# Performance work log

Measured on AMD Instinct MI355X. Metric: run time of the kernel, lower is better.

The kernel has to match this reference:

```python
import jax, jax.numpy as jnp
import numpy as np

B, N, E = 4, 1024, 16
S = 4  # num species
AH = PH = 64  # hidden dims


def _mlp(x, W0, b0, W1, b1, W2, b2):
    h = jax.nn.silu(x @ W0 + b0)
    h = jax.nn.silu(h @ W1 + b1)
    return h @ W2 + b2  # [..., 1]


def setup_inputs() -> dict:
    key = jax.random.key(0)
    ks = jax.random.split(key, 20)
    scale = 0.1
    inp = {
        "positions": jax.random.normal(ks[0], (B, N, 2), jnp.float32),
        "species": jax.random.randint(ks[1], (B, N), 0, S, jnp.int32),
        "electric_field": jax.random.normal(ks[2], (B, 2), jnp.float32),
        "embed": jax.random.normal(ks[3], (S, E), jnp.float32) * scale,
        "aW0": jax.random.normal(ks[4], (2 + 2 + 1 + E, AH), jnp.float32) * scale,
        "ab0": jax.random.normal(ks[5], (AH,), jnp.float32) * scale,
        "aW1": jax.random.normal(ks[6], (AH, AH), jnp.float32) * scale,
        "ab1": jax.random.normal(ks[7], (AH,), jnp.float32) * scale,
        "aW2": jax.random.normal(ks[8], (AH, 1), jnp.float32) * scale,
        "ab2": jax.random.normal(ks[9], (1,), jnp.float32) * scale,
        "pW0": jax.random.normal(ks[10], (2 + 1 + 1 + 1 + 2 * E, PH), jnp.float32) * scale,
        "pb0": jax.random.normal(ks[11], (PH,), jnp.float32) * scale,
        "pW1": jax.random.normal(ks[12], (PH, PH), jnp.float32) * scale,
        "pb1": jax.random.normal(ks[13], (PH,), jnp.float32) * scale,
        "pW2": jax.random.normal(ks[14], (PH, 1), jnp.float32) * scale,
        "pb2": jax.random.normal(ks[15], (1,), jnp.float32) * scale,
    }
    return inp


def reference(positions, species, electric_field, embed,
              aW0, ab0, aW1, ab1, aW2, ab2,
              pW0, pb0, pW1, pb1, pW2, pb2):
    num_atoms = positions.shape[1]
    cp = positions - positions.mean(axis=1, keepdims=True)         # [B,N,2]
    semb = embed[species]                                          # [B,N,E]
    e_norm = jnp.linalg.norm(electric_field, axis=-1, keepdims=True)  # [B,1]

    # atom channel
    atom_field = jnp.broadcast_to(electric_field[:, None, :], (cp.shape[0], num_atoms, 2))
    atom_enorm = jnp.broadcast_to(e_norm[:, None, :], (cp.shape[0], num_atoms, 1))
    atom_feat = jnp.concatenate([cp, atom_field, atom_enorm, semb], axis=-1)
    atom_energy = _mlp(atom_feat, aW0, ab0, aW1, ab1, aW2, ab2)[..., 0].sum(axis=1)

    # pair channel: all i<j pairs, fully vectorized
    i_idx, j_idx = jnp.triu_indices(num_atoms, k=1)                # [P]
    rij = cp[:, i_idx, :] - cp[:, j_idx, :]                        # [B,P,2]
    dij = jnp.linalg.norm(rij, axis=-1, keepdims=True)             # [B,P,1]
    uij = rij / jnp.maximum(dij, 1e-12)
    e_dot_u = jnp.sum(electric_field[:, None, :] * uij, axis=-1, keepdims=True)
    pair_enorm = jnp.broadcast_to(e_norm[:, None, :], dij.shape)
    pair_feat = jnp.concatenate(
        [rij, dij, e_dot_u, pair_enorm, semb[:, i_idx, :], semb[:, j_idx, :]], axis=-1)
    pair_energy = _mlp(pair_feat, pW0, pb0, pW1, pb1, pW2, pb2)[..., 0].sum(axis=1)

    return atom_energy + pair_energy
```

## Files before the change

kernel.cpp:

```cpp
#include <hip/hip_runtime.h>

#define NA 1024
#define NBATCH 4
#define NPAIR 523776
#define PAIR_TILES 2046
#define PAIR_BLOCKS 512
#define GRID_X 513

#define WS_MEAN 0
#define WS_W0P  64
#define WS_W0A  4160
#define WS_W1P  8256
#define WS_W1A  16448

typedef _Float16 half8 __attribute__((ext_vector_type(8)));
typedef float float4v __attribute__((ext_vector_type(4)));

__device__ __forceinline__ float silu_f(float x) {
    return x * __builtin_amdgcn_rcpf(1.0f + __expf(-x));
}

__device__ __forceinline__ uint32_t pkf16(float a, float b) {
    union { _Float16 h[2]; uint32_t u; } x;
    x.h[0] = (_Float16)a; x.h[1] = (_Float16)b;
    return x.u;
}

__global__ void prep_kernel(const float* __restrict__ positions,
                            const float* __restrict__ embed,
                            const float* __restrict__ aW0,
                            const float* __restrict__ ab0,
                            const float* __restrict__ aW1,
                            const float* __restrict__ ab2,
                            const float* __restrict__ pW0,
                            const float* __restrict__ pb0,
                            const float* __restrict__ pW1,
                            const float* __restrict__ pb2,
                            char* __restrict__ ws,
                            float* __restrict__ out) {
    const int tid = threadIdx.x;
    if (blockIdx.x < 4) {
        const int b = blockIdx.x;
        const float2* pos = (const float2*)positions + b * NA;
        float sx = 0.f, sy = 0.f;
        for (int t = tid; t < NA; t += 256) {
            float2 p = pos[t];
            sx += p.x; sy += p.y;
        }
#pragma unroll
        for (int off = 32; off > 0; off >>= 1) {
            sx += __shfl_down(sx, off);
            sy += __shfl_down(sy, off);
        }
        __shared__ float rxs[4], rys[4];
        const int w = tid >> 6, lane = tid & 63;
        if (lane == 0) { rxs[w] = sx; rys[w] = sy; }
        __syncthreads();
        if (tid == 0) {
            float* meanws = (float*)(ws + WS_MEAN);
            meanws[b * 2 + 0] = (rxs[0] + rxs[1] + rxs[2] + rxs[3]) * (1.f / NA);
            meanws[b * 2 + 1] = (rys[0] + rys[1] + rys[2] + rys[3]) * (1.f / NA);
            out[b] = (float)NPAIR * pb2[0] + (float)NA * ab2[0];
        }
        return;
    }

    _Float16* w0p = (_Float16*)(ws + WS_W0P);
    _Float16* w0a = (_Float16*)(ws + WS_W0A);
    _Float16* w1p = (_Float16*)(ws + WS_W1P);
    _Float16* w1a = (_Float16*)(ws + WS_W1A);

    for (int idx = tid; idx < 2048; idx += 256) {
        const int j = idx & 7, lane = (idx >> 3) & 63, nt = idx >> 9;
        const int k = ((lane >> 4) << 3) + j;
        const int col = nt * 16 + (lane & 15);
        float vp = 0.f, va = 0.f;
        if (k < 5) {
            vp = pW0[k * 64 + col];
            va = aW0[k * 64 + col];
        } else if (k == 5) {
            vp = pb0[col];
            va = ab0[col];
        } else if (k >= 6 && k <= 9) {
            const int s = k - 6;
            float accp = 0.f, acca = 0.f;
#pragma unroll
            for (int e = 0; e < 16; e++) {
                float em = embed[s * 16 + e];
                accp += em * pW0[(5 + e) * 64 + col];
                acca += em * aW0[(5 + e) * 64 + col];
            }
            vp = accp; va = acca;
        } else if (k >= 10 && k <= 13) {
            const int s = k - 10;
            float accp = 0.f;
#pragma unroll
            for (int e = 0; e < 16; e++)
                accp += embed[s * 16 + e] * pW0[(21 + e) * 64 + col];
            vp = accp; va = 0.f;
        }
        w0p[idx] = (_Float16)vp;
        w0a[idx] = (_Float16)va;
    }
    for (int idx = tid; idx < 4096; idx += 256) {
        const int j = idx & 7, lane = (idx >> 3) & 63;
        const int ks = (idx >> 9) & 1, nt = idx >> 10;
        const int q = lane >> 4;
        const int m = (j < 4) ? (4 * q + j) : (16 + 4 * q + (j - 4));
        const int k = ks * 32 + m;
        const int col = nt * 16 + (lane & 15);
        w1p[idx] = (_Float16)pW1[k * 64 + col];
        w1a[idx] = (_Float16)aW1[k * 64 + col];
    }
}

__global__ __launch_bounds__(256, 4) void mlp_kernel(
    const float* __restrict__ positions,
    const int*   __restrict__ species,
    const float* __restrict__ efield,
    const float* __restrict__ ab1, const float* __restrict__ aW2,
    const float* __restrict__ pb1, const float* __restrict__ pW2,
    const char*  __restrict__ ws,
    float* __restrict__ out)
{
    const int b    = blockIdx.y;
    const int bx   = blockIdx.x;
    const bool is_atom = (bx == PAIR_BLOCKS);
    const int tid  = threadIdx.x;
    const int lane = tid & 63;
    const int wv   = tid >> 6;
    const int n16  = lane & 15;
    const int quad = lane >> 4;

    __shared__ __attribute__((aligned(16))) _Float16 Xbuf[4][64][40];
    _Float16 (*rows)[40] = Xbuf[wv];

    const _Float16* w0w = (const _Float16*)(ws + (is_atom ? WS_W0A : WS_W0P));
    const _Float16* w1w = (const _Float16*)(ws + (is_atom ? WS_W1A : WS_W1P));
    half8 w0f[4], w1f[4][2];
#pragma unroll
    for (int nt = 0; nt < 4; nt++)
        w0f[nt] = *(const half8*)(w0w + (nt * 64 + lane) * 8);
#pragma unroll
    for (int nt = 0; nt < 4; nt++)
#pragma unroll
        for (int ks = 0; ks < 2; ks++)
            w1f[nt][ks] = *(const half8*)(w1w + ((nt * 2 + ks) * 64 + lane) * 8);

    const float* B1 = is_atom ? ab1 : pb1;
    const float* W2 = is_atom ? aW2 : pW2;
    float4v b1q[4], w2q[4];
#pragma unroll
    for (int nt = 0; nt < 4; nt++) {
        b1q[nt] = *(const float4v*)(B1 + nt * 16 + quad * 4);
        w2q[nt] = *(const float4v*)(W2 + nt * 16 + quad * 4);
    }

    *(int4*)&rows[lane][16] = make_int4(0, 0, 0, 0);
    *(int4*)&rows[lane][24] = make_int4(0, 0, 0, 0);

    const float Ex = efield[b * 2 + 0];
    const float Ey = efield[b * 2 + 1];
    const float enorm = sqrtf(Ex * Ex + Ey * Ey);
    const float* meanws = (const float*)(ws + WS_MEAN);

    const int my_tiles = is_atom ? 4 : ((bx < PAIR_TILES - 3 * PAIR_BLOCKS) ? 4 : 3);

    float energy = 0.f;
    for (int t = 0; t < my_tiles; ++t) {
        float f0, f1, f2, f3;
        uint64_t ohi, ohj;
        if (!is_atom) {
            const int tile = bx + t * PAIR_BLOCKS;
            const int p = tile * 256 + tid;
            float Df = (float)(2047 * 2047 - 8 * p);
            int i = (int)((2047.0f - sqrtf(Df)) * 0.5f);
            i = i < 0 ? 0 : (i > 1022 ? 1022 : i);
            while (i * (2047 - i) / 2 > p) --i;
            while ((i + 1) * (2046 - i) / 2 <= p) ++i;
            const int j = p - i * (2047 - i) / 2 + i + 1;
            const float2* pos = (const float2*)positions + b * NA;
            float2 pi = pos[i], pj = pos[j];
            f0 = pi.x - pj.x; f1 = pi.y - pj.y;
            f2 = sqrtf(f0 * f0 + f1 * f1);
            float inv = __builtin_amdgcn_rcpf(fmaxf(f2, 1e-12f));
            f3 = (Ex * f0 + Ey * f1) * inv;
            ohi = 0x3C00ull << (species[b * NA + i] * 16);
            ohj = 0x3C00ull << (species[b * NA + j] * 16);
        } else {
            const int n = t * 256 + tid;
            float2 pn = ((const float2*)positions)[b * NA + n];
            f0 = pn.x - meanws[b * 2 + 0];
            f1 = pn.y - meanws[b * 2 + 1];
            f2 = Ex; f3 = Ey;
            ohi = 0x3C00ull << (species[b * NA + n] * 16);
            ohj = 0;
        }
        int4* dst = (int4*)&rows[lane][0];
        int4 lo, hi;
        lo.x = (int)pkf16(f0, f1);
        lo.y = (int)pkf16(f2, f3);
        lo.z = (int)pkf16(enorm, 1.0f);
        lo.w = (int)(uint32_t)ohi;
        hi.x = (int)(uint32_t)(ohi >> 32);
        hi.y = (int)(uint32_t)ohj;
        hi.z = (int)(uint32_t)(ohj >> 32);
        hi.w = 0;
        dst[0] = lo;
        dst[1] = hi;

#pragma unroll
        for (int mt = 0; mt < 4; mt++) {
            half8 xf = *(const half8*)(&rows[mt * 16 + n16][quad * 8]);

            float4v acc[4];
#pragma unroll
            for (int nt = 0; nt < 4; nt++) {
                float4v z = {0.f, 0.f, 0.f, 0.f};
                acc[nt] = __builtin_amdgcn_mfma_f32_16x16x32_f16(w0f[nt], xf, z, 0, 0, 0);
            }
            half8 h0, h1;
#pragma unroll
            for (int r = 0; r < 4; r++) {
                h0[r]     = (_Float16)silu_f(acc[0][r]);
                h0[4 + r] = (_Float16)silu_f(acc[1][r]);
                h1[r]     = (_Float16)silu_f(acc[2][r]);
                h1[4 + r] = (_Float16)silu_f(acc[3][r]);
            }

#pragma unroll
            for (int nt = 0; nt < 4; nt++) {
                float4v c = b1q[nt];
                c = __builtin_amdgcn_mfma_f32_16x16x32_f16(w1f[nt][0], h0, c, 0, 0, 0);
                c = __builtin_amdgcn_mfma_f32_16x16x32_f16(w1f[nt][1], h1, c, 0, 0, 0);
#pragma unroll
                for (int r = 0; r < 4; r++)
                    energy += silu_f(c[r]) * w2q[nt][r];
            }
        }
    }

#pragma unroll
    for (int off = 32; off > 0; off >>= 1)
        energy += __shfl_down(energy, off);
    __shared__ float wsum[4];
    if (lane == 0) wsum[wv] = energy;
    __syncthreads();
    if (tid == 0)
        atomicAdd(&out[b], wsum[0] + wsum[1] + wsum[2] + wsum[3]);
}

extern "C" void kernel_launch(void* const* d_in, const int* in_sizes, int n_in,
                              void* d_out, int out_size, void* d_ws, size_t ws_size,
                              hipStream_t stream) {
    const float* positions = (const float*)d_in[0];
    const int*   species   = (const int*)  d_in[1];
    const float* efield    = (const float*)d_in[2];
    const float* embed     = (const float*)d_in[3];
    const float* aW0 = (const float*)d_in[4];
    const float* ab0 = (const float*)d_in[5];
    const float* aW1 = (const float*)d_in[6];
    const float* ab1 = (const float*)d_in[7];
    const float* aW2 = (const float*)d_in[8];
    const float* ab2 = (const float*)d_in[9];
    const float* pW0 = (const float*)d_in[10];
    const float* pb0 = (const float*)d_in[11];
    const float* pW1 = (const float*)d_in[12];
    const float* pb1 = (const float*)d_in[13];
    const float* pW2 = (const float*)d_in[14];
    const float* pb2 = (const float*)d_in[15];
    float* outp = (float*)d_out;
    char*  ws   = (char*)d_ws;

    prep_kernel<<<dim3(5), dim3(256), 0, stream>>>(
        positions, embed, aW0, ab0, aW1, ab2, pW0, pb0, pW1, pb2, ws, outp);
    mlp_kernel<<<dim3(GRID_X, NBATCH), dim3(256), 0, stream>>>(
        positions, species, efield,
        ab1, aW2, pb1, pW2,
        ws, outp);
}
```

Before: 169.2 us.

## Shrink layer-0 MFMA to K=16, fold log2e into weights, defer W2 dot

Packs the 14 layer-0 input features into a K=16 fragment and uses the 16x16x16 f16 MFMA, halving layer-0 matrix work, shared-memory row width and weight-prep size. Folds log2(e) into the layer-0 weights and layer-1 bias so SiLU can use a raw exp2, then undoes the scale with ln2 at the end. Defers the multiply by W2 until after the tile loop: each thread keeps per-column SiLU sums and does one dot product at the end, dropping per-element FMAs and registers. The pair grid shrinks to 511 blocks, so two blocks now take 5 tiles instead of 4, which may lengthen the tail; occupancy is pinned with amdgpu_waves_per_eu.

```diff
diff --git a/kernel.cpp b/kernel.cpp
--- a/kernel.cpp
+++ b/kernel.cpp
@@ -4,20 +4,33 @@
 #define NBATCH 4
 #define NPAIR 523776
 #define PAIR_TILES 2046
-#define PAIR_BLOCKS 512
-#define GRID_X 513
+#define PAIR_BLOCKS 511
+#define GRID_X 512
+
+#define LOG2E_F 1.44269504088896f
+#define LN2_F   0.69314718055995f
 
 #define WS_MEAN 0
 #define WS_W0P  64
-#define WS_W0A  4160
-#define WS_W1P  8256
-#define WS_W1A  16448
-
+#define WS_W0A  2112
+#define WS_W1P  4160
+#define WS_W1A  12352
+
+typedef _Float16 half4 __attribute__((ext_vector_type(4)));
 typedef _Float16 half8 __attribute__((ext_vector_type(8)));
 typedef float float4v __attribute__((ext_vector_type(4)));
 
-__device__ __forceinline__ float silu_f(float x) {
-    return x * __builtin_amdgcn_rcpf(1.0f + __expf(-x));
+#if defined(__has_builtin)
+#  if __has_builtin(__builtin_amdgcn_exp2f)
+#    define EXP2F(x) __builtin_amdgcn_exp2f(x)
+#  endif
+#endif
+#ifndef EXP2F
+#  define EXP2F(x) exp2f(x)
+#endif
+
+__device__ __forceinline__ float siluy(float y) {
+    return y * __builtin_amdgcn_rcpf(1.0f + EXP2F(-y));
 }
 
 __device__ __forceinline__ uint32_t pkf16(float a, float b) {
@@ -70,9 +83,9 @@
     _Float16* w1p = (_Float16*)(ws + WS_W1P);
     _Float16* w1a = (_Float16*)(ws + WS_W1A);
 
-    for (int idx = tid; idx < 2048; idx += 256) {
-        const int j = idx & 7, lane = (idx >> 3) & 63, nt = idx >> 9;
-        const int k = ((lane >> 4) << 3) + j;
+    for (int idx = tid; idx < 1024; idx += 256) {
+        const int j = idx & 3, lane = (idx >> 2) & 63, nt = idx >> 8;
+        const int k = ((lane >> 4) << 2) + j;
         const int col = nt * 16 + (lane & 15);
         float vp = 0.f, va = 0.f;
         if (k < 5) {
@@ -99,8 +112,8 @@
                 accp += embed[s * 16 + e] * pW0[(21 + e) * 64 + col];
             vp = accp; va = 0.f;
         }
-        w0p[idx] = (_Float16)vp;
-        w0a[idx] = (_Float16)va;
+        w0p[idx] = (_Float16)(vp * LOG2E_F);
+        w0a[idx] = (_Float16)(va * LOG2E_F);
     }
     for (int idx = tid; idx < 4096; idx += 256) {
         const int j = idx & 7, lane = (idx >> 3) & 63;
@@ -114,7 +127,9 @@
     }
 }
 
-__global__ __launch_bounds__(256, 4) void mlp_kernel(
+__global__ __launch_bounds__(256)
+__attribute__((amdgpu_waves_per_eu(4, 4)))
+void mlp_kernel(
     const float* __restrict__ positions,
     const int*   __restrict__ species,
     const float* __restrict__ efield,
@@ -132,15 +147,16 @@
     const int n16  = lane & 15;
     const int quad = lane >> 4;
 
-    __shared__ __attribute__((aligned(16))) _Float16 Xbuf[4][64][40];
-    _Float16 (*rows)[40] = Xbuf[wv];
+    __shared__ __attribute__((aligned(16))) _Float16 Xbuf[4][64][24];
+    _Float16 (*rows)[24] = Xbuf[wv];
 
     const _Float16* w0w = (const _Float16*)(ws + (is_atom ? WS_W0A : WS_W0P));
     const _Float16* w1w = (const _Float16*)(ws + (is_atom ? WS_W1A : WS_W1P));
-    half8 w0f[4], w1f[4][2];
+    half4 w0f[4];
+    half8 w1f[4][2];
 #pragma unroll
     for (int nt = 0; nt < 4; nt++)
-        w0f[nt] = *(const half8*)(w0w + (nt * 64 + lane) * 8);
+        w0f[nt] = *(const half4*)(w0w + (nt * 64 + lane) * 4);
 #pragma unroll
     for (int nt = 0; nt < 4; nt++)
 #pragma unroll
@@ -148,25 +164,25 @@
             w1f[nt][ks] = *(const half8*)(w1w + ((nt * 2 + ks) * 64 + lane) * 8);
 
     const float* B1 = is_atom ? ab1 : pb1;
-    const float* W2 = is_atom ? aW2 : pW2;
-    float4v b1q[4], w2q[4];
+    float4v b1q[4];
 #pragma unroll
     for (int nt = 0; nt < 4; nt++) {
-        b1q[nt] = *(const float4v*)(B1 + nt * 16 + quad * 4);
-        w2q[nt] = *(const float4v*)(W2 + nt * 16 + quad * 4);
-    }
-
-    *(int4*)&rows[lane][16] = make_int4(0, 0, 0, 0);
-    *(int4*)&rows[lane][24] = make_int4(0, 0, 0, 0);
+        float4v t4 = *(const float4v*)(B1 + nt * 16 + quad * 4);
+        b1q[nt] = t4 * LOG2E_F;
+    }
 
     const float Ex = efield[b * 2 + 0];
     const float Ey = efield[b * 2 + 1];
     const float enorm = sqrtf(Ex * Ex + Ey * Ey);
     const float* meanws = (const float*)(ws + WS_MEAN);
 
-    const int my_tiles = is_atom ? 4 : ((bx < PAIR_TILES - 3 * PAIR_BLOCKS) ? 4 : 3);
-
-    float energy = 0.f;
+    const int my_tiles = is_atom ? 4 : ((bx < PAIR_TILES - 4 * PAIR_BLOCKS) ? 5 : 4);
+
+    const float4v zero4 = {0.f, 0.f, 0.f, 0.f};
+    float4v acce[4];
+#pragma unroll
+    for (int nt = 0; nt < 4; nt++) acce[nt] = zero4;
+
     for (int t = 0; t < my_tiles; ++t) {
         float f0, f1, f2, f3;
         uint64_t ohi, ohj;
@@ -209,23 +225,26 @@
         dst[0] = lo;
         dst[1] = hi;
 
+        half4 xfr[4];
+#pragma unroll
+        for (int mt = 0; mt < 4; mt++)
+            xfr[mt] = *(const half4*)(&rows[mt * 16 + n16][quad * 4]);
+
 #pragma unroll
         for (int mt = 0; mt < 4; mt++) {
-            half8 xf = *(const half8*)(&rows[mt * 16 + n16][quad * 8]);
-
             float4v acc[4];
 #pragma unroll
-            for (int nt = 0; nt < 4; nt++) {
-                float4v z = {0.f, 0.f, 0.f, 0.f};
-                acc[nt] = __builtin_amdgcn_mfma_f32_16x16x32_f16(w0f[nt], xf, z, 0, 0, 0);
-            }
+            for (int nt = 0; nt < 4; nt++)
+                acc[nt] = __builtin_amdgcn_mfma_f32_16x16x16f16(
+                    w0f[nt], xfr[mt], zero4, 0, 0, 0);
+
             half8 h0, h1;
 #pragma unroll
             for (int r = 0; r < 4; r++) {
-                h0[r]     = (_Float16)silu_f(acc[0][r]);
-                h0[4 + r] = (_Float16)silu_f(acc[1][r]);
-                h1[r]     = (_Float16)silu_f(acc[2][r]);
-                h1[4 + r] = (_Float16)silu_f(acc[3][r]);
+                h0[r]     = (_Float16)siluy(acc[0][r]);
+                h0[4 + r] = (_Float16)siluy(acc[1][r]);
+                h1[r]     = (_Float16)siluy(acc[2][r]);
+                h1[4 + r] = (_Float16)siluy(acc[3][r]);
             }
 
 #pragma unroll
@@ -235,10 +254,21 @@
                 c = __builtin_amdgcn_mfma_f32_16x16x32_f16(w1f[nt][1], h1, c, 0, 0, 0);
 #pragma unroll
                 for (int r = 0; r < 4; r++)
-                    energy += silu_f(c[r]) * w2q[nt][r];
+                    acce[nt][r] += siluy(c[r]);
             }
         }
     }
+
+    const float* W2 = is_atom ? aW2 : pW2;
+    float dot = 0.f;
+#pragma unroll
+    for (int nt = 0; nt < 4; nt++) {
+        float4v w2v4 = *(const float4v*)(W2 + nt * 16 + quad * 4);
+#pragma unroll
+        for (int r = 0; r < 4; r++)
+            dot += acce[nt][r] * w2v4[r];
+    }
+    float energy = dot * LN2_F;
 
 #pragma unroll
     for (int off = 32; off > 0; off >>= 1)
```

New measurement: 151.1 us. 1.12x faster.
